# Optimization experiments

Hardware: AMD Instinct MI355X
Metric: run time of the kernel (lower is better)

The kernel has to match this reference:

```python
import jax, jax.numpy as jnp
import numpy as np

TOP_K = 8

def setup_inputs() -> dict:
    key = jax.random.key(0)
    k1, k2 = jax.random.split(key)
    hidden_states = jax.random.normal(k1, (4, 4096, 2048), dtype=jnp.float32)
    weight = jax.random.normal(k2, (64, 2048), dtype=jnp.float32) * 0.02
    return {"hidden_states": hidden_states, "weight": weight}

def reference(hidden_states, weight):
    b, s, h = hidden_states.shape
    x = hidden_states.reshape(-1, h).astype(jnp.float32)   # [T, H]
    logits = jnp.einsum('th,eh->te', x, weight.astype(jnp.float32))  # [T, E]
    scores = jax.nn.softmax(logits, axis=-1)               # greedy router: softmax then top-k
    topk_weights, topk_idx = jax.lax.top_k(scores, TOP_K)  # [T, k]
    # renormalize top-k probabilities (norm_topk_prob)
    topk_weights = topk_weights / jnp.sum(topk_weights, axis=-1, keepdims=True)
    return topk_weights, topk_idx
```

## Files before the change

kernel.cpp:

```cpp
#include <hip/hip_runtime.h>
#include <math.h>


#define H_DIM 2048
#define N_EXP 64
#define TOPK 8
#define TOK 32
#define NSTEP 16

typedef __attribute__((ext_vector_type(8))) short bf16x8;
typedef __attribute__((ext_vector_type(4))) float f32x4;

union FragU { uint4 q; unsigned u[4]; bf16x8 s; };

__device__ inline unsigned cvt_pk_bf16(float lo, float hi) {
  unsigned d;
  asm("v_cvt_pk_bf16_f32 %0, %1, %2" : "=v"(d) : "v"(lo), "v"(hi));
  return d;
}

__device__ inline void split3(const float* e, unsigned* dh, unsigned* dm,
                              unsigned* dl) {
#pragma unroll
  for (int p = 0; p < 4; ++p) {
    const float f0 = e[2 * p], f1 = e[2 * p + 1];
    const unsigned h = cvt_pk_bf16(f0, f1);
    const float r0 = f0 - __uint_as_float(h << 16);
    const float r1 = f1 - __uint_as_float(h & 0xffff0000u);
    const unsigned m = cvt_pk_bf16(r0, r1);
    const float s0 = r0 - __uint_as_float(m << 16);
    const float s1 = r1 - __uint_as_float(m & 0xffff0000u);
    dl[p] = cvt_pk_bf16(s0, s1);
    dh[p] = h;
    dm[p] = m;
  }
}

__global__ __launch_bounds__(256) void w_split_kernel(
    const float* __restrict__ w, uint4* __restrict__ ws) {
  const int id = blockIdx.x * 256 + threadIdx.x;
  const int l = id & 63;
  const int nt = (id >> 6) & 3;
  const int ksg = id >> 8;
  const int n = nt * 16 + (l & 15);
  const int kb = ksg * 32 + ((l >> 4) << 3);
  const float* wr = w + (size_t)n * H_DIM + kb;
  const float4 a = *(const float4*)(wr);
  const float4 b = *(const float4*)(wr + 4);
  const float e[8] = {a.x, a.y, a.z, a.w, b.x, b.y, b.z, b.w};
  unsigned dh[4], dm[4], dl[4];
  split3(e, dh, dm, dl);
  const int base = (ksg * 12 + nt * 3) * 64 + l;
  ws[base] = make_uint4(dh[0], dh[1], dh[2], dh[3]);
  ws[base + 64] = make_uint4(dm[0], dm[1], dm[2], dm[3]);
  ws[base + 128] = make_uint4(dl[0], dl[1], dl[2], dl[3]);
}

__device__ __forceinline__ void load_b6(uint4 (&dst)[6], const uint4* wb,
                                        int off) {
#pragma unroll
  for (int i = 0; i < 6; ++i) dst[i] = wb[(off + i) * 64];
}

__device__ __forceinline__ void load_x2(float4 (&dst)[2], const float* p) {
  dst[0] = *(const float4*)(p);
  dst[1] = *(const float4*)(p + 4);
}

__device__ __forceinline__ void mfma_half(const bf16x8& ah, const bf16x8& am,
                                          const bf16x8& al,
                                          const uint4 (&bfr)[6],
                                          f32x4 (&acc)[4], int nt0) {
#pragma unroll
  for (int j = 0; j < 2; ++j) {
    FragU bh, bm, bl;
    bh.q = bfr[j * 3 + 0];
    bm.q = bfr[j * 3 + 1];
    bl.q = bfr[j * 3 + 2];
    f32x4 c = acc[nt0 + j];
    c = __builtin_amdgcn_mfma_f32_16x16x32_bf16(ah, bh.s, c, 0, 0, 0);
    c = __builtin_amdgcn_mfma_f32_16x16x32_bf16(am, bh.s, c, 0, 0, 0);
    c = __builtin_amdgcn_mfma_f32_16x16x32_bf16(ah, bm.s, c, 0, 0, 0);
    c = __builtin_amdgcn_mfma_f32_16x16x32_bf16(al, bh.s, c, 0, 0, 0);
    c = __builtin_amdgcn_mfma_f32_16x16x32_bf16(ah, bl.s, c, 0, 0, 0);
    c = __builtin_amdgcn_mfma_f32_16x16x32_bf16(am, bm.s, c, 0, 0, 0);
    acc[nt0 + j] = c;
  }
}

__global__ __launch_bounds__(512, 2) void moe_gate_kernel(
    const float* __restrict__ x, const uint4* __restrict__ wf_g,
    float* __restrict__ out, int n_tokens) {
  __shared__ float part[8 * 1024];
  __shared__ float logits[N_EXP * TOK];

  const int tid = threadIdx.x;
  const int l = tid & 63;
  const int w = tid >> 6;
  const int tp = w & 1;
  const int kq = w >> 1;
  const int t0 = blockIdx.x * TOK;

  const float* xp =
      x + (size_t)(t0 + tp * 16 + (l & 15)) * H_DIM + kq * 512 + ((l >> 4) << 3);
  const uint4* wbase = wf_g + (size_t)(kq * 16) * 768 + l;

  f32x4 acc[4];
#pragma unroll
  for (int nt = 0; nt < 4; ++nt) acc[nt] = (f32x4){0.f, 0.f, 0.f, 0.f};

  uint4 bA[6], bB[6];
  float4 xA[2], xB[2], xC[2];

  load_b6(bA, wbase, 0);
  load_b6(bB, wbase, 6);
  load_x2(xA, xp);
  load_x2(xB, xp + 32);

#pragma unroll 1
  for (int s = 0; s < NSTEP; ++s) {
    bf16x8 ah, am, al;
    {
      const float4 v0 = xA[0], v1 = xA[1];
      const float e[8] = {v0.x, v0.y, v0.z, v0.w, v1.x, v1.y, v1.z, v1.w};
      FragU uh, um, ul;
      split3(e, uh.u, um.u, ul.u);
      ah = uh.s;
      am = um.s;
      al = ul.s;
    }
    mfma_half(ah, am, al, bA, acc, 0);
    if (s + 1 < NSTEP) load_b6(bA, wbase + (size_t)(s + 1) * 768, 0);
    if (s + 2 < NSTEP) load_x2(xC, xp + (s + 2) * 32);
    mfma_half(ah, am, al, bB, acc, 2);
    if (s + 1 < NSTEP) load_b6(bB, wbase + (size_t)(s + 1) * 768, 6);
    xA[0] = xB[0]; xA[1] = xB[1];
    xB[0] = xC[0]; xB[1] = xC[1];
  }

#pragma unroll
  for (int nt = 0; nt < 4; ++nt)
    *(float4*)&part[w * 1024 + nt * 256 + l * 4] =
        make_float4(acc[nt][0], acc[nt][1], acc[nt][2], acc[nt][3]);
  __syncthreads();

  for (int z = tid; z < N_EXP * TOK; z += 512) {
    const int e = z >> 5, t32 = z & 31;
    const int tpz = t32 >> 4, r16 = t32 & 15;
    const int q = r16 >> 2, rz = r16 & 3;
    const int idx = (e >> 4) * 256 + (q * 16 + (e & 15)) * 4 + rz;
    float v = ((part[(0 * 2 + tpz) * 1024 + idx] +
                part[(1 * 2 + tpz) * 1024 + idx]) +
               (part[(2 * 2 + tpz) * 1024 + idx] +
                part[(3 * 2 + tpz) * 1024 + idx]));
    logits[z] = v;
  }
  __syncthreads();

  if (tid >= TOK) return;

  float lg[N_EXP];
#pragma unroll
  for (int e = 0; e < N_EXP; ++e) lg[e] = logits[e * TOK + tid];

  float bw[TOPK];
  int bi[TOPK];
#pragma unroll
  for (int k = 0; k < TOPK; ++k) {
    float m = lg[0];
    int mi = 0;
#pragma unroll
    for (int e = 1; e < N_EXP; ++e) {
      if (lg[e] > m) {
        m = lg[e];
        mi = e;
      }
    }
    bw[k] = m;
    bi[k] = mi;
#pragma unroll
    for (int e = 0; e < N_EXP; ++e)
      if (e == mi) lg[e] = -INFINITY;
  }

  const float mx = bw[0];
  float ew[TOPK];
  float s = 0.f;
#pragma unroll
  for (int k = 0; k < TOPK; ++k) {
    ew[k] = expf(bw[k] - mx);
    s += ew[k];
  }
  const float inv = 1.f / s;

  float4 w0, w1, i0, i1;
  w0.x = ew[0] * inv; w0.y = ew[1] * inv; w0.z = ew[2] * inv; w0.w = ew[3] * inv;
  w1.x = ew[4] * inv; w1.y = ew[5] * inv; w1.z = ew[6] * inv; w1.w = ew[7] * inv;
  i0.x = (float)bi[0]; i0.y = (float)bi[1]; i0.z = (float)bi[2]; i0.w = (float)bi[3];
  i1.x = (float)bi[4]; i1.y = (float)bi[5]; i1.z = (float)bi[6]; i1.w = (float)bi[7];

  const int t = t0 + tid;
  float4* ow = reinterpret_cast<float4*>(out + (size_t)t * TOPK);
  ow[0] = w0;
  ow[1] = w1;
  float4* oi =
      reinterpret_cast<float4*>(out + (size_t)n_tokens * TOPK + (size_t)t * TOPK);
  oi[0] = i0;
  oi[1] = i1;
}

extern "C" void kernel_launch(void* const* d_in, const int* in_sizes, int n_in,
                              void* d_out, int out_size, void* d_ws,
                              size_t ws_size, hipStream_t stream) {
  const float* x = (const float*)d_in[0];
  const float* w = (const float*)d_in[1];
  float* out = (float*)d_out;
  const int n_tokens = in_sizes[0] / H_DIM;
  w_split_kernel<<<64, 256, 0, stream>>>(w, (uint4*)d_ws);
  const int n_blocks = n_tokens / TOK;
  moe_gate_kernel<<<n_blocks, 512, 0, stream>>>(x, (const uint4*)d_ws, out,
                                                n_tokens);
}
```

Measured before the change: 226.8 us.

## Stage weight fragments in LDS and split experts across waves instead of K

The work split changes from four waves each handling a quarter of K for all 64 experts to each wave owning one 16-expert tile over the full K. Split-bf16 weight fragments are shared across waves by staging them into double-buffered LDS with global_load_lds, synchronised by barriers. This drops the cross-wave partial-sum reduction through shared memory and reduces redundant weight loads per block. The cost is a block barrier every iteration and LDS traffic, and each wave now runs a single dependent MFMA accumulation chain.

```diff
diff --git a/kernel.cpp b/kernel.cpp
--- a/kernel.cpp
+++ b/kernel.cpp
@@ -6,7 +6,7 @@
 #define N_EXP 64
 #define TOPK 8
 #define TOK 32
-#define NSTEP 16
+#define NIT 32
 
 typedef __attribute__((ext_vector_type(8))) short bf16x8;
 typedef __attribute__((ext_vector_type(4))) float f32x4;
@@ -56,105 +56,100 @@
   ws[base + 128] = make_uint4(dl[0], dl[1], dl[2], dl[3]);
 }
 
-__device__ __forceinline__ void load_b6(uint4 (&dst)[6], const uint4* wb,
-                                        int off) {
-#pragma unroll
-  for (int i = 0; i < 6; ++i) dst[i] = wb[(off + i) * 64];
-}
-
-__device__ __forceinline__ void load_x2(float4 (&dst)[2], const float* p) {
-  dst[0] = *(const float4*)(p);
-  dst[1] = *(const float4*)(p + 4);
-}
-
-__device__ __forceinline__ void mfma_half(const bf16x8& ah, const bf16x8& am,
-                                          const bf16x8& al,
-                                          const uint4 (&bfr)[6],
-                                          f32x4 (&acc)[4], int nt0) {
-#pragma unroll
-  for (int j = 0; j < 2; ++j) {
-    FragU bh, bm, bl;
-    bh.q = bfr[j * 3 + 0];
-    bm.q = bfr[j * 3 + 1];
-    bl.q = bfr[j * 3 + 2];
-    f32x4 c = acc[nt0 + j];
-    c = __builtin_amdgcn_mfma_f32_16x16x32_bf16(ah, bh.s, c, 0, 0, 0);
-    c = __builtin_amdgcn_mfma_f32_16x16x32_bf16(am, bh.s, c, 0, 0, 0);
-    c = __builtin_amdgcn_mfma_f32_16x16x32_bf16(ah, bm.s, c, 0, 0, 0);
-    c = __builtin_amdgcn_mfma_f32_16x16x32_bf16(al, bh.s, c, 0, 0, 0);
-    c = __builtin_amdgcn_mfma_f32_16x16x32_bf16(ah, bl.s, c, 0, 0, 0);
-    c = __builtin_amdgcn_mfma_f32_16x16x32_bf16(am, bm.s, c, 0, 0, 0);
-    acc[nt0 + j] = c;
-  }
-}
-
 __global__ __launch_bounds__(512, 2) void moe_gate_kernel(
     const float* __restrict__ x, const uint4* __restrict__ wf_g,
     float* __restrict__ out, int n_tokens) {
-  __shared__ float part[8 * 1024];
+  __shared__ char bstage[2 * 24576];
   __shared__ float logits[N_EXP * TOK];
 
   const int tid = threadIdx.x;
   const int l = tid & 63;
   const int w = tid >> 6;
-  const int tp = w & 1;
-  const int kq = w >> 1;
+  const int m = __builtin_amdgcn_readfirstlane(w & 1);
+  const int n4 = __builtin_amdgcn_readfirstlane(w >> 1);
   const int t0 = blockIdx.x * TOK;
 
   const float* xp =
-      x + (size_t)(t0 + tp * 16 + (l & 15)) * H_DIM + kq * 512 + ((l >> 4) << 3);
-  const uint4* wbase = wf_g + (size_t)(kq * 16) * 768 + l;
-
-  f32x4 acc[4];
-#pragma unroll
-  for (int nt = 0; nt < 4; ++nt) acc[nt] = (f32x4){0.f, 0.f, 0.f, 0.f};
-
-  uint4 bA[6], bB[6];
-  float4 xA[2], xB[2], xC[2];
-
-  load_b6(bA, wbase, 0);
-  load_b6(bB, wbase, 6);
-  load_x2(xA, xp);
-  load_x2(xB, xp + 32);
+      x + (size_t)(t0 + m * 16 + (l & 15)) * H_DIM + ((l >> 4) << 3);
+  const char* wsb = (const char*)wf_g;
+
+  auto stage = [&](int ii) {
+    const char* src = wsb + (size_t)ii * 24576 + w * 3072 + l * 16;
+    char* dst = bstage + (ii & 1) * 24576 + w * 3072;
+#pragma unroll
+    for (int j = 0; j < 3; ++j)
+      __builtin_amdgcn_global_load_lds(
+          (const __attribute__((address_space(1))) void*)(src + j * 1024),
+          (__attribute__((address_space(3))) void*)(dst + j * 1024), 16, 0, 0);
+  };
+
+  auto load_x4 = [&](float4(&dst)[4], int i) {
+    const float* p = xp + i * 64;
+    dst[0] = *(const float4*)(p);
+    dst[1] = *(const float4*)(p + 4);
+    dst[2] = *(const float4*)(p + 32);
+    dst[3] = *(const float4*)(p + 36);
+  };
+
+  f32x4 acc = (f32x4){0.f, 0.f, 0.f, 0.f};
+  float4 xA[4], xB[4], xC[4];
+
+  stage(0);
+  __builtin_amdgcn_sched_barrier(0);
+  load_x4(xA, 0);
+  load_x4(xB, 1);
+  asm volatile("s_waitcnt vmcnt(8)" ::: "memory");
+  __builtin_amdgcn_s_barrier();
 
 #pragma unroll 1
-  for (int s = 0; s < NSTEP; ++s) {
-    bf16x8 ah, am, al;
-    {
-      const float4 v0 = xA[0], v1 = xA[1];
-      const float e[8] = {v0.x, v0.y, v0.z, v0.w, v1.x, v1.y, v1.z, v1.w};
-      FragU uh, um, ul;
-      split3(e, uh.u, um.u, ul.u);
-      ah = uh.s;
-      am = um.s;
-      al = ul.s;
-    }
-    mfma_half(ah, am, al, bA, acc, 0);
-    if (s + 1 < NSTEP) load_b6(bA, wbase + (size_t)(s + 1) * 768, 0);
-    if (s + 2 < NSTEP) load_x2(xC, xp + (s + 2) * 32);
-    mfma_half(ah, am, al, bB, acc, 2);
-    if (s + 1 < NSTEP) load_b6(bB, wbase + (size_t)(s + 1) * 768, 6);
-    xA[0] = xB[0]; xA[1] = xB[1];
-    xB[0] = xC[0]; xB[1] = xC[1];
-  }
-
-#pragma unroll
-  for (int nt = 0; nt < 4; ++nt)
-    *(float4*)&part[w * 1024 + nt * 256 + l * 4] =
-        make_float4(acc[nt][0], acc[nt][1], acc[nt][2], acc[nt][3]);
+  for (int i = 0; i < NIT; ++i) {
+    if (i + 1 < NIT) stage(i + 1);
+    __builtin_amdgcn_sched_barrier(0);
+    if (i + 2 < NIT) load_x4(xC, i + 2);
+
+    const char* lb = bstage + (i & 1) * 24576 + (n4 * 3) * 1024 + l * 16;
+#pragma unroll
+    for (int kk = 0; kk < 2; ++kk) {
+      bf16x8 ah, am, al;
+      {
+        const float4 v0 = xA[kk * 2], v1 = xA[kk * 2 + 1];
+        const float e[8] = {v0.x, v0.y, v0.z, v0.w, v1.x, v1.y, v1.z, v1.w};
+        FragU uh, um, ul;
+        split3(e, uh.u, um.u, ul.u);
+        ah = uh.s;
+        am = um.s;
+        al = ul.s;
+      }
+      FragU bh, bm, bl;
+      bh.q = *(const uint4*)(lb + kk * 12288 + 0);
+      bm.q = *(const uint4*)(lb + kk * 12288 + 1024);
+      bl.q = *(const uint4*)(lb + kk * 12288 + 2048);
+      acc = __builtin_amdgcn_mfma_f32_16x16x32_bf16(ah, bh.s, acc, 0, 0, 0);
+      acc = __builtin_amdgcn_mfma_f32_16x16x32_bf16(am, bh.s, acc, 0, 0, 0);
+      acc = __builtin_amdgcn_mfma_f32_16x16x32_bf16(ah, bm.s, acc, 0, 0, 0);
+      acc = __builtin_amdgcn_mfma_f32_16x16x32_bf16(al, bh.s, acc, 0, 0, 0);
+      acc = __builtin_amdgcn_mfma_f32_16x16x32_bf16(ah, bl.s, acc, 0, 0, 0);
+      acc = __builtin_amdgcn_mfma_f32_16x16x32_bf16(am, bm.s, acc, 0, 0, 0);
+    }
+
+#pragma unroll
+    for (int j = 0; j < 4; ++j) {
+      xA[j] = xB[j];
+      xB[j] = xC[j];
+    }
+
+    if (i + 1 < NIT) {
+      if (i + 2 < NIT)
+        asm volatile("s_waitcnt vmcnt(4)" ::: "memory");
+      else
+        asm volatile("s_waitcnt vmcnt(0)" ::: "memory");
+      __builtin_amdgcn_s_barrier();
+    }
+  }
+
   __syncthreads();
-
-  for (int z = tid; z < N_EXP * TOK; z += 512) {
-    const int e = z >> 5, t32 = z & 31;
-    const int tpz = t32 >> 4, r16 = t32 & 15;
-    const int q = r16 >> 2, rz = r16 & 3;
-    const int idx = (e >> 4) * 256 + (q * 16 + (e & 15)) * 4 + rz;
-    float v = ((part[(0 * 2 + tpz) * 1024 + idx] +
-                part[(1 * 2 + tpz) * 1024 + idx]) +
-               (part[(2 * 2 + tpz) * 1024 + idx] +
-                part[(3 * 2 + tpz) * 1024 + idx]));
-    logits[z] = v;
-  }
+  *(float4*)&logits[(n4 * 16 + (l & 15)) * TOK + m * 16 + ((l >> 4) << 2)] =
+      make_float4(acc[0], acc[1], acc[2], acc[3]);
   __syncthreads();
 
   if (tid >= TOK) return;
@@ -167,16 +162,16 @@
   int bi[TOPK];
 #pragma unroll
   for (int k = 0; k < TOPK; ++k) {
-    float m = lg[0];
+    float mx_ = lg[0];
     int mi = 0;
 #pragma unroll
     for (int e = 1; e < N_EXP; ++e) {
-      if (lg[e] > m) {
-        m = lg[e];
+      if (lg[e] > mx_) {
+        mx_ = lg[e];
         mi = e;
       }
     }
-    bw[k] = m;
+    bw[k] = mx_;
     bi[k] = mi;
 #pragma unroll
     for (int e = 0; e < N_EXP; ++e)
```

New measurement: 236.7 us. 4.4% more time.
